# Performance work log

Measured on AMD Instinct MI355X. Metric: run time of the kernel, lower is better.

Reference implementation:

```python
import jax, jax.numpy as jnp
import numpy as np

EMB = 768
HEADS = 3
HD = EMB // HEADS  # 256
B, S = 4, 2048


def setup_inputs() -> dict:
    key = jax.random.key(0)
    ks = jax.random.split(key, 8)
    inputs_for_keys = jax.random.normal(ks[0], (B, S, EMB), dtype=jnp.float32)
    inputs_for_values = jax.random.normal(ks[1], (B, S, EMB), dtype=jnp.float32)
    inputs_for_queries = jax.random.normal(ks[2], (B, S, EMB), dtype=jnp.float32)
    # stacked per-head projection weights: [heads, emb, head_dim]
    # original uses 'random_uniform' init (small uniform); scale ~0.05
    Wk = jax.random.uniform(ks[3], (HEADS, EMB, HD), jnp.float32, -0.05, 0.05)
    Wv = jax.random.uniform(ks[4], (HEADS, EMB, HD), jnp.float32, -0.05, 0.05)
    Wq = jax.random.uniform(ks[5], (HEADS, EMB, HD), jnp.float32, -0.05, 0.05)
    Wo = jax.random.normal(ks[6], (EMB, EMB), dtype=jnp.float32) * (1.0 / np.sqrt(EMB))
    bo = jnp.zeros((EMB,), dtype=jnp.float32)
    return {
        "inputs_for_keys": inputs_for_keys,
        "inputs_for_values": inputs_for_values,
        "inputs_for_queries": inputs_for_queries,
        "Wk": Wk, "Wv": Wv, "Wq": Wq, "Wo": Wo, "bo": bo,
    }


def reference(inputs_for_keys, inputs_for_values, inputs_for_queries, Wk, Wv, Wq, Wo, bo):
    # per-head projections, batched over heads: [b, h, s, f]
    K = jnp.einsum('bse,hef->bhsf', inputs_for_keys, Wk)
    V = jnp.einsum('bse,hef->bhsf', inputs_for_values, Wv)
    Q = jnp.einsum('bse,hef->bhsf', inputs_for_queries, Wq)

    seq_k = inputs_for_keys.shape[1]
    seq_q = inputs_for_queries.shape[1]
    # NOTE: original scales by sqrt(window_size_keys) (seq len), not sqrt(d_k)
    scale = jnp.sqrt(jnp.float32(seq_k))

    scores = jnp.einsum('bhqf,bhkf->bhqk', Q, K) / scale
    # causal mask: -inf strictly above the diagonal (j > i)
    mask = jnp.triu(jnp.full((seq_q, seq_k), -jnp.inf, dtype=scores.dtype), k=1)
    scores = scores + mask

    attn = jax.nn.softmax(scores, axis=-1)  # [b,h,q,k]
    heads = jnp.einsum('bhqk,bhkf->bhqf', attn, V)

    # concat heads along feature dim: [b, q, heads*hd]
    b, h, q, f = heads.shape
    concat = heads.transpose(0, 2, 1, 3).reshape(b, q, h * f)
    return concat @ Wo + bo
```

## Files before the change

### kernel.cpp

```cpp
#include <hip/hip_runtime.h>

#define BATCH 4
#define NHEADS 3
#define SEQ 2048
#define HDIM 256
#define EMBD 768
#define MTOT (BATCH*SEQ)
#define WSZ (NHEADS*EMBD*HDIM)

typedef unsigned short u16x8 __attribute__((ext_vector_type(8)));
typedef unsigned short u16x4 __attribute__((ext_vector_type(4)));
typedef __bf16 bf16x8 __attribute__((ext_vector_type(8)));
typedef float fx4 __attribute__((ext_vector_type(4)));

__device__ __forceinline__ unsigned short f2bf(float x) {
    union { float f; unsigned int u; } v; v.f = x;
    unsigned int r = v.u + 0x7fffu + ((v.u >> 16) & 1u);
    return (unsigned short)(r >> 16);
}

__device__ __forceinline__ fx4 mfma16(u16x8 a, u16x8 b, fx4 c) {
    return __builtin_amdgcn_mfma_f32_16x16x32_bf16(
        __builtin_bit_cast(bf16x8, a), __builtin_bit_cast(bf16x8, b), c, 0, 0, 0);
}

__device__ __forceinline__ void gl_lds16(const unsigned short* g, unsigned short* l) {
    __builtin_amdgcn_global_load_lds(
        (const __attribute__((address_space(1))) unsigned int*)g,
        (__attribute__((address_space(3))) unsigned int*)l, 16, 0, 0);
}

__device__ const unsigned char attn_sched[48] = {
    124,125, 63, 120,121, 116,117, 59, 112,113, 108,109, 55, 104,105,
    100,101, 51,  96, 97,  92, 93, 47,  88, 89,  84, 85, 43,  80, 81,
     76, 77, 39,  72, 73,  68, 69, 35,  64, 65,  31, 27, 23, 19, 15,
     11,  7,  3
};

__global__ __launch_bounds__(256) void castAw_kernel(
    const float* __restrict__ Ak, const float* __restrict__ Av,
    const float* __restrict__ Aq,
    const float* __restrict__ Wk, const float* __restrict__ Wv,
    const float* __restrict__ Wq, const float* __restrict__ Wo,
    unsigned short* __restrict__ Abf, unsigned short* __restrict__ Wt,
    unsigned short* __restrict__ Wot)
{
    __shared__ float tile[64][65];
    int bx = blockIdx.x;
    if (bx < 9216) {
        int e = (bx * 256 + threadIdx.x) * 8;
        int t = e / (MTOT * EMBD);
        int r = e - t * (MTOT * EMBD);
        const float* A = (t == 0) ? Ak : (t == 1) ? Av : Aq;
        const fx4* s = (const fx4*)(A + r);
        fx4 v0 = s[0], v1 = s[1];
        u16x8 o;
        o[0]=f2bf(v0[0]); o[1]=f2bf(v0[1]); o[2]=f2bf(v0[2]); o[3]=f2bf(v0[3]);
        o[4]=f2bf(v1[0]); o[5]=f2bf(v1[1]); o[6]=f2bf(v1[2]); o[7]=f2bf(v1[3]);
        *(u16x8*)(Abf + e) = o;
        return;
    }
    int z = bx - 9216;
    const float* src; unsigned short* dst;
    int src_ld, dst_ld, e0, f0;
    if (z < 432) {
        int t = z / 144, rem = z - t * 144;
        int h = rem / 48, tl = rem - h * 48;
        e0 = (tl % 12) * 64; f0 = (tl / 12) * 64;
        const float* W = (t == 0) ? Wk : (t == 1) ? Wv : Wq;
        src = W + h * 768 * 256; src_ld = 256;
        dst = Wt + t * WSZ + h * 256 * 768; dst_ld = 768;
    } else {
        int zz = z - 432;
        e0 = (zz % 12) * 64; f0 = (zz / 12) * 64;
        src = Wo; src_ld = 768;
        dst = Wot; dst_ld = 768;
    }
    int tx = threadIdx.x & 63, ty4 = threadIdx.x >> 6;
    #pragma unroll
    for (int i = 0; i < 16; ++i) {
        int r = ty4 + i * 4;
        tile[r][tx] = src[(e0 + r) * src_ld + f0 + tx];
    }
    __syncthreads();
    #pragma unroll
    for (int i = 0; i < 16; ++i) {
        int r = ty4 + i * 4;
        dst[(f0 + r) * dst_ld + e0 + tx] = f2bf(tile[tx][r]);
    }
}

__global__ __launch_bounds__(256) void proj_kernel(
    const unsigned short* __restrict__ Abf, const unsigned short* __restrict__ Wt,
    unsigned short* __restrict__ Kg, unsigned short* __restrict__ Vg,
    unsigned short* __restrict__ Qg)
{
    __shared__ alignas(16) unsigned short S[17408];
    unsigned short* As = S;
    unsigned short* Bs = S + 8192;

    int z = blockIdx.z;
    const unsigned short* A = Abf + z * (MTOT * EMBD);
    int m0 = blockIdx.x * 128;
    int h = blockIdx.y >> 1, fbase = (blockIdx.y & 1) * 128;
    const unsigned short* W = Wt + z * WSZ + (h * 256 + fbase) * EMBD;

    int tid = threadIdx.x;
    int w = tid >> 6, ln = tid & 63;
    int lane16 = ln & 15, quad = ln >> 4;
    int mw = (w & 1) * 64, nw = (w >> 1) * 64;

    fx4 acc[4][4];
    #pragma unroll
    for (int i = 0; i < 4; ++i)
        #pragma unroll
        for (int j = 0; j < 4; ++j) acc[i][j] = (fx4){0.f, 0.f, 0.f, 0.f};

    int c0 = tid, c1 = tid + 256;
    int r0 = c0 >> 2, s0_ = (c0 & 3) * 8;
    int r1 = c1 >> 2, s1_ = (c1 & 3) * 8;
    const unsigned short* Ag0 = A + (m0 + r0) * EMBD + s0_;
    const unsigned short* Ag1 = A + (m0 + r1) * EMBD + s1_;
    const unsigned short* Wg0 = W + r0 * EMBD + s0_;
    const unsigned short* Wg1 = W + r1 * EMBD + s1_;

    for (int kb = 0; kb < EMBD; kb += 32) {
        __syncthreads();
        gl_lds16(Ag0 + kb, &As[c0 * 8]);
        gl_lds16(Ag1 + kb, &As[c1 * 8]);
        gl_lds16(Wg0 + kb, &Bs[c0 * 8]);
        gl_lds16(Wg1 + kb, &Bs[c1 * 8]);
        __syncthreads();

        u16x8 af[4], bf[4];
        #pragma unroll
        for (int i = 0; i < 4; ++i) {
            af[i] = *(const u16x8*)&As[(mw + i * 16 + lane16) * 32 + quad * 8];
            bf[i] = *(const u16x8*)&Bs[(nw + i * 16 + lane16) * 32 + quad * 8];
        }
        #pragma unroll
        for (int i = 0; i < 4; ++i)
            #pragma unroll
            for (int j = 0; j < 4; ++j)
                acc[i][j] = mfma16(af[i], bf[j], acc[i][j]);
    }

    __syncthreads();
    int b = m0 >> 11, sq0 = m0 & 2047;

    if (z == 1) {
        #pragma unroll
        for (int i = 0; i < 4; ++i)
            #pragma unroll
            for (int j = 0; j < 4; ++j) {
                int fl = nw + j * 16 + lane16;
                int ml = mw + i * 16 + quad * 4;
                u16x4 pk;
                pk[0] = f2bf(acc[i][j][0]); pk[1] = f2bf(acc[i][j][1]);
                pk[2] = f2bf(acc[i][j][2]); pk[3] = f2bf(acc[i][j][3]);
                *(u16x4*)&S[fl * 136 + ml] = pk;
            }
        __syncthreads();
        int fl = tid >> 1, mseg = (tid & 1) * 64;
        const unsigned short* srcp = &S[fl * 136 + mseg];
        unsigned short* dstp = Vg + ((b * NHEADS + h) * HDIM + fbase + fl) * SEQ + sq0 + mseg;
        #pragma unroll
        for (int c = 0; c < 8; ++c)
            *(u16x8*)(dstp + c * 8) = *(const u16x8*)(srcp + c * 8);
    } else {
        #pragma unroll
        for (int i = 0; i < 4; ++i)
            #pragma unroll
            for (int j = 0; j < 4; ++j) {
                int fl = nw + j * 16 + lane16;
                int ml = mw + i * 16 + quad * 4;
                #pragma unroll
                for (int r = 0; r < 4; ++r)
                    S[(ml + r) * 136 + fl] = f2bf(acc[i][j][r]);
            }
        __syncthreads();
        unsigned short* dst0 = (z == 0) ? Kg : Qg;
        int ml = tid >> 1, fseg = (tid & 1) * 64;
        const unsigned short* srcp = &S[ml * 136 + fseg];
        unsigned short* dstp = dst0 + ((b * NHEADS + h) * SEQ + sq0 + ml) * HDIM + fbase + fseg;
        #pragma unroll
        for (int c = 0; c < 8; ++c)
            *(u16x8*)(dstp + c * 8) = *(const u16x8*)(srcp + c * 8);
    }
}

__global__ __launch_bounds__(256) void attn_kernel(
    const unsigned short* __restrict__ Kg, const unsigned short* __restrict__ Vg,
    const unsigned short* __restrict__ Qg, unsigned short* __restrict__ heads,
    float* __restrict__ Opart, float* __restrict__ Lpart)
{
    __shared__ alignas(16) unsigned short Ks[32 * 264];
    __shared__ alignas(16) unsigned short Vs[256 * 40];

    int bx = blockIdx.x;
    int bh = bx % 12;
    int ent = attn_sched[bx / 12];
    int qt = ent >> 2, kc = ent & 3;
    int tid = threadIdx.x;
    int w = tid >> 6, ln = tid & 63;
    int lane16 = ln & 15, quad = ln >> 4;
    int q0w = qt * 64 + w * 16;

    const unsigned short* Kbase = Kg + bh * (SEQ * HDIM);
    const unsigned short* Vbase = Vg + bh * (SEQ * HDIM);
    const unsigned short* Qbase = Qg + bh * (SEQ * HDIM);

    u16x8 qf[8];
    {
        const unsigned short* qrow = Qbase + (q0w + lane16) * HDIM + quad * 8;
        #pragma unroll
        for (int c = 0; c < 8; ++c) qf[c] = *(const u16x8*)(qrow + c * 32);
    }

    fx4 o[16];
    #pragma unroll
    for (int i = 0; i < 16; ++i) o[i] = (fx4){0.f, 0.f, 0.f, 0.f};
    float lsum = 0.f;

    const float Cs2 = 0.03188010519640429f;

    int t0, t1;
    if (kc == 3) { t0 = 0; t1 = 2 * qt + 2; }
    else         { t0 = kc * (qt + 1); t1 = t0 + qt + 1; }

    int ksrow = tid >> 3, kseg = tid & 7;
    const unsigned short* kstage = Kbase + ksrow * HDIM + kseg * 32;
    const unsigned short* vstage = Vbase + tid * SEQ;

    u16x8 kreg[4], vreg[4];
    {
        int k0 = t0 * 32;
        #pragma unroll
        for (int j = 0; j < 4; ++j) {
            kreg[j] = *(const u16x8*)(kstage + k0 * HDIM + j * 8);
            vreg[j] = *(const u16x8*)(vstage + k0 + j * 8);
        }
    }

    for (int kt = t0; kt < t1; ++kt) {
        __syncthreads();
        {
            u16x8* kd = (u16x8*)&Ks[ksrow * 264 + kseg * 32];
            kd[0] = kreg[0]; kd[1] = kreg[1]; kd[2] = kreg[2]; kd[3] = kreg[3];
            u16x8* vd = (u16x8*)&Vs[tid * 40];
            vd[0] = vreg[0]; vd[1] = vreg[1]; vd[2] = vreg[2]; vd[3] = vreg[3];
        }
        if (kt + 1 < t1) {
            int k0n = (kt + 1) * 32;
            #pragma unroll
            for (int j = 0; j < 4; ++j) {
                kreg[j] = *(const u16x8*)(kstage + k0n * HDIM + j * 8);
                vreg[j] = *(const u16x8*)(vstage + k0n + j * 8);
            }
        }
        __syncthreads();

        int k0 = kt * 32;
        fx4 s0 = (fx4){0.f,0.f,0.f,0.f}, s1 = (fx4){0.f,0.f,0.f,0.f};
        #pragma unroll
        for (int c = 0; c < 8; ++c) {
            u16x8 ka = *(const u16x8*)&Ks[lane16 * 264 + c * 32 + quad * 8];
            u16x8 kb = *(const u16x8*)&Ks[(16 + lane16) * 264 + c * 32 + quad * 8];
            s0 = mfma16(ka, qf[c], s0);
            s1 = mfma16(kb, qf[c], s1);
        }

        float p0[4], p1[4];
        int q = q0w + lane16;
        #pragma unroll
        for (int r = 0; r < 4; ++r) {
            int ka_ = k0 + quad * 4 + r;
            float e0 = exp2f(s0[r] * Cs2);
            float e1 = exp2f(s1[r] * Cs2);
            p0[r] = (ka_      <= q) ? e0 : 0.f;
            p1[r] = (ka_ + 16 <= q) ? e1 : 0.f;
            lsum += p0[r] + p1[r];
        }

        u16x8 pf;
        #pragma unroll
        for (int j = 0; j < 8; ++j) {
            int srcLane = ((((quad << 1) + (j >> 2)) & 3) << 4) | lane16;
            float v0 = __shfl(p0[j & 3], srcLane, 64);
            float v1 = __shfl(p1[j & 3], srcLane, 64);
            pf[j] = f2bf(quad >= 2 ? v1 : v0);
        }

        #pragma unroll
        for (int ft = 0; ft < 16; ++ft) {
            u16x8 vf = *(const u16x8*)&Vs[(ft * 16 + lane16) * 40 + quad * 8];
            o[ft] = mfma16(pf, vf, o[ft]);
        }
    }

    lsum += __shfl_xor(lsum, 16, 64);
    lsum += __shfl_xor(lsum, 32, 64);

    if (kc == 3) {
        float linv = 1.f / lsum;
        float inv[4];
        #pragma unroll
        for (int r = 0; r < 4; ++r) inv[r] = __shfl(linv, quad * 4 + r, 64);
        int b = bh / 3, h = bh - (bh / 3) * 3;
        unsigned short* hp = heads + (b * SEQ + q0w + quad * 4) * EMBD + h * HDIM + lane16;
        #pragma unroll
        for (int ft = 0; ft < 16; ++ft)
            #pragma unroll
            for (int r = 0; r < 4; ++r)
                hp[r * EMBD + ft * 16] = f2bf(o[ft][r] * inv[r]);
    } else {
        int slot = (bh * 16 + (qt - 16)) * 2 + kc;
        float* Op = Opart + slot * 16384 + (w * 16 + quad * 4) * 256 + lane16;
        #pragma unroll
        for (int ft = 0; ft < 16; ++ft)
            #pragma unroll
            for (int r = 0; r < 4; ++r)
                Op[r * 256 + ft * 16] = o[ft][r];
        if (quad == 0) Lpart[slot * 64 + w * 16 + lane16] = lsum;
    }
}

__global__ __launch_bounds__(256) void combine_kernel(
    const float* __restrict__ Opart, const float* __restrict__ Lpart,
    unsigned short* __restrict__ heads)
{
    int t = blockIdx.x;
    int bh = t >> 4, qt = (t & 15) + 16;
    int s0 = t * 2, s1 = s0 + 1;
    int tid = threadIdx.x;
    int row = tid >> 2, fseg = (tid & 3) * 64;
    float l = Lpart[s0 * 64 + row] + Lpart[s1 * 64 + row];
    float inv = 1.f / l;
    const fx4* O0 = (const fx4*)(Opart + s0 * 16384 + row * 256 + fseg);
    const fx4* O1 = (const fx4*)(Opart + s1 * 16384 + row * 256 + fseg);
    int b = bh / 3, h = bh - (bh / 3) * 3;
    unsigned short* hp = heads + (b * SEQ + qt * 64 + row) * EMBD + h * HDIM + fseg;
    #pragma unroll
    for (int i = 0; i < 16; ++i) {
        fx4 v = O0[i] + O1[i];
        u16x4 pk;
        pk[0] = f2bf(v[0] * inv); pk[1] = f2bf(v[1] * inv);
        pk[2] = f2bf(v[2] * inv); pk[3] = f2bf(v[3] * inv);
        *(u16x4*)(hp + i * 4) = pk;
    }
}

__global__ __launch_bounds__(256) void outproj_kernel(
    const unsigned short* __restrict__ A, const unsigned short* __restrict__ Wot,
    const float* __restrict__ bo, float* __restrict__ out)
{
    __shared__ alignas(16) unsigned short S[16384];
    unsigned short* As = S;
    unsigned short* Bs = S + 8192;

    int m0 = blockIdx.x * 128, n0 = blockIdx.y * 128;
    int tid = threadIdx.x;
    int w = tid >> 6, ln = tid & 63;
    int lane16 = ln & 15, quad = ln >> 4;
    int mw = (w & 1) * 64, nw = (w >> 1) * 64;

    fx4 acc[4][4];
    #pragma unroll
    for (int i = 0; i < 4; ++i)
        #pragma unroll
        for (int j = 0; j < 4; ++j) acc[i][j] = (fx4){0.f, 0.f, 0.f, 0.f};

    int c0 = tid, c1 = tid + 256;
    int r0 = c0 >> 2, s0_ = (c0 & 3) * 8;
    int r1 = c1 >> 2, s1_ = (c1 & 3) * 8;
    const unsigned short* Ag0 = A + (m0 + r0) * EMBD + s0_;
    const unsigned short* Ag1 = A + (m0 + r1) * EMBD + s1_;
    const unsigned short* Wg0 = Wot + (n0 + r0) * EMBD + s0_;
    const unsigned short* Wg1 = Wot + (n0 + r1) * EMBD + s1_;

    for (int kb = 0; kb < EMBD; kb += 32) {
        __syncthreads();
        gl_lds16(Ag0 + kb, &As[c0 * 8]);
        gl_lds16(Ag1 + kb, &As[c1 * 8]);
        gl_lds16(Wg0 + kb, &Bs[c0 * 8]);
        gl_lds16(Wg1 + kb, &Bs[c1 * 8]);
        __syncthreads();

        u16x8 af[4], bf[4];
        #pragma unroll
        for (int i = 0; i < 4; ++i) {
            af[i] = *(const u16x8*)&As[(mw + i * 16 + lane16) * 32 + quad * 8];
            bf[i] = *(const u16x8*)&Bs[(nw + i * 16 + lane16) * 32 + quad * 8];
        }
        #pragma unroll
        for (int i = 0; i < 4; ++i)
            #pragma unroll
            for (int j = 0; j < 4; ++j)
                acc[i][j] = mfma16(af[i], bf[j], acc[i][j]);
    }

    #pragma unroll
    for (int i = 0; i < 4; ++i) {
        int mb = m0 + mw + i * 16 + quad * 4;
        #pragma unroll
        for (int j = 0; j < 4; ++j) {
            int n = n0 + nw + j * 16 + lane16;
            float bias = bo[n];
            #pragma unroll
            for (int r = 0; r < 4; ++r)
                out[(mb + r) * EMBD + n] = acc[i][j][r] + bias;
        }
    }
}

extern "C" void kernel_launch(void* const* d_in, const int* in_sizes, int n_in,
                              void* d_out, int out_size, void* d_ws, size_t ws_size,
                              hipStream_t stream) {
    const float* Ak = (const float*)d_in[0];
    const float* Av = (const float*)d_in[1];
    const float* Aq = (const float*)d_in[2];
    const float* Wk = (const float*)d_in[3];
    const float* Wv = (const float*)d_in[4];
    const float* Wq = (const float*)d_in[5];
    const float* Wo = (const float*)d_in[6];
    const float* bo = (const float*)d_in[7];
    float* out = (float*)d_out;

    char* base = (char*)d_ws;
    unsigned short* Wt    = (unsigned short*)(base);
    unsigned short* Wot   = (unsigned short*)(base + 3538944);
    unsigned short* Abf   = (unsigned short*)(base + 4718592);
    unsigned short* Kg    = (unsigned short*)(base + 42467328);
    unsigned short* Vg    = (unsigned short*)(base + 55050240);
    unsigned short* Qg    = (unsigned short*)(base + 67633152);
    unsigned short* heads = (unsigned short*)(base + 80216064);
    float* Opart = (float*)(base + 4718592);
    float* Lpart = (float*)(base + 4718592 + 25165824);

    castAw_kernel<<<dim3(9792), dim3(256), 0, stream>>>(
        Ak, Av, Aq, Wk, Wv, Wq, Wo, Abf, Wt, Wot);
    proj_kernel<<<dim3(64, 6, 3), dim3(256), 0, stream>>>(
        Abf, Wt, Kg, Vg, Qg);
    attn_kernel<<<dim3(576), dim3(256), 0, stream>>>(
        Kg, Vg, Qg, heads, Opart, Lpart);
    combine_kernel<<<dim3(192), dim3(256), 0, stream>>>(Opart, Lpart, heads);
    outproj_kernel<<<dim3(64, 6), dim3(256), 0, stream>>>(heads, Wot, bo, out);
}
```

Baseline: 292.8 us.

## Use 64-key tiles with direct global-to-LDS loads in attention kernel

Doubles the key/value tile per iteration from 32 to 64 and drops the register-staged prefetch in favour of direct global-to-LDS loads (gl_lds16) into unpadded shared arrays. The causal tile ranges and the split between partial chunks are recomputed for the larger tile. The aim is fewer barriers per key and less VGPR staging traffic. In exchange it loses the overlap between the next tile's loads and current compute, and the unpadded 512-byte and 128-byte LDS row strides may cause bank conflicts on fragment reads.

```diff
diff --git a/kernel.cpp b/kernel.cpp
--- a/kernel.cpp
+++ b/kernel.cpp
@@ -194,8 +194,8 @@
     const unsigned short* __restrict__ Qg, unsigned short* __restrict__ heads,
     float* __restrict__ Opart, float* __restrict__ Lpart)
 {
-    __shared__ alignas(16) unsigned short Ks[32 * 264];
-    __shared__ alignas(16) unsigned short Vs[256 * 40];
+    __shared__ alignas(16) unsigned short Ks[64 * 256];
+    __shared__ alignas(16) unsigned short Vs[256 * 64];
 
     int bx = blockIdx.x;
     int bh = bx % 12;
@@ -225,76 +225,65 @@
     const float Cs2 = 0.03188010519640429f;
 
     int t0, t1;
-    if (kc == 3) { t0 = 0; t1 = 2 * qt + 2; }
-    else         { t0 = kc * (qt + 1); t1 = t0 + qt + 1; }
-
-    int ksrow = tid >> 3, kseg = tid & 7;
-    const unsigned short* kstage = Kbase + ksrow * HDIM + kseg * 32;
-    const unsigned short* vstage = Vbase + tid * SEQ;
-
-    u16x8 kreg[4], vreg[4];
-    {
-        int k0 = t0 * 32;
-        #pragma unroll
-        for (int j = 0; j < 4; ++j) {
-            kreg[j] = *(const u16x8*)(kstage + k0 * HDIM + j * 8);
-            vreg[j] = *(const u16x8*)(vstage + k0 + j * 8);
+    if (kc == 3) { t0 = 0; t1 = qt + 1; }
+    else         { int half = (qt + 1) >> 1;
+                   t0 = kc ? half : 0; t1 = kc ? qt + 1 : half; }
+
+    const unsigned short* kgp = Kbase + (tid >> 5) * HDIM + (tid & 31) * 8;
+    const unsigned short* vgp = Vbase + (tid >> 3) * SEQ + (tid & 7) * 8;
+    unsigned short* ksl = &Ks[tid * 8];
+    unsigned short* vsl = &Vs[tid * 8];
+
+    for (int kt = t0; kt < t1; ++kt) {
+        int k0 = kt * 64;
+        __syncthreads();
+        #pragma unroll
+        for (int j = 0; j < 8; ++j)
+            gl_lds16(kgp + (k0 + j * 8) * HDIM, ksl + j * 2048);
+        #pragma unroll
+        for (int j = 0; j < 8; ++j)
+            gl_lds16(vgp + j * 32 * SEQ + k0, vsl + j * 2048);
+        __syncthreads();
+
+        fx4 sacc[4];
+        #pragma unroll
+        for (int ks = 0; ks < 4; ++ks) sacc[ks] = (fx4){0.f,0.f,0.f,0.f};
+        #pragma unroll
+        for (int c = 0; c < 8; ++c) {
+            #pragma unroll
+            for (int ks = 0; ks < 4; ++ks) {
+                u16x8 kf = *(const u16x8*)&Ks[(ks * 16 + lane16) * 256 + c * 32 + quad * 8];
+                sacc[ks] = mfma16(kf, qf[c], sacc[ks]);
+            }
         }
-    }
-
-    for (int kt = t0; kt < t1; ++kt) {
-        __syncthreads();
-        {
-            u16x8* kd = (u16x8*)&Ks[ksrow * 264 + kseg * 32];
-            kd[0] = kreg[0]; kd[1] = kreg[1]; kd[2] = kreg[2]; kd[3] = kreg[3];
-            u16x8* vd = (u16x8*)&Vs[tid * 40];
-            vd[0] = vreg[0]; vd[1] = vreg[1]; vd[2] = vreg[2]; vd[3] = vreg[3];
-        }
-        if (kt + 1 < t1) {
-            int k0n = (kt + 1) * 32;
-            #pragma unroll
-            for (int j = 0; j < 4; ++j) {
-                kreg[j] = *(const u16x8*)(kstage + k0n * HDIM + j * 8);
-                vreg[j] = *(const u16x8*)(vstage + k0n + j * 8);
-            }
-        }
-        __syncthreads();
-
-        int k0 = kt * 32;
-        fx4 s0 = (fx4){0.f,0.f,0.f,0.f}, s1 = (fx4){0.f,0.f,0.f,0.f};
-        #pragma unroll
-        for (int c = 0; c < 8; ++c) {
-            u16x8 ka = *(const u16x8*)&Ks[lane16 * 264 + c * 32 + quad * 8];
-            u16x8 kb = *(const u16x8*)&Ks[(16 + lane16) * 264 + c * 32 + quad * 8];
-            s0 = mfma16(ka, qf[c], s0);
-            s1 = mfma16(kb, qf[c], s1);
-        }
-
-        float p0[4], p1[4];
+
+        float p[4][4];
         int q = q0w + lane16;
         #pragma unroll
-        for (int r = 0; r < 4; ++r) {
-            int ka_ = k0 + quad * 4 + r;
-            float e0 = exp2f(s0[r] * Cs2);
-            float e1 = exp2f(s1[r] * Cs2);
-            p0[r] = (ka_      <= q) ? e0 : 0.f;
-            p1[r] = (ka_ + 16 <= q) ? e1 : 0.f;
-            lsum += p0[r] + p1[r];
-        }
-
-        u16x8 pf;
-        #pragma unroll
-        for (int j = 0; j < 8; ++j) {
-            int srcLane = ((((quad << 1) + (j >> 2)) & 3) << 4) | lane16;
-            float v0 = __shfl(p0[j & 3], srcLane, 64);
-            float v1 = __shfl(p1[j & 3], srcLane, 64);
-            pf[j] = f2bf(quad >= 2 ? v1 : v0);
-        }
-
-        #pragma unroll
-        for (int ft = 0; ft < 16; ++ft) {
-            u16x8 vf = *(const u16x8*)&Vs[(ft * 16 + lane16) * 40 + quad * 8];
-            o[ft] = mfma16(pf, vf, o[ft]);
+        for (int ks = 0; ks < 4; ++ks)
+            #pragma unroll
+            for (int r = 0; r < 4; ++r) {
+                int ka_ = k0 + ks * 16 + quad * 4 + r;
+                float e = exp2f(sacc[ks][r] * Cs2);
+                p[ks][r] = (ka_ <= q) ? e : 0.f;
+                lsum += p[ks][r];
+            }
+
+        #pragma unroll
+        for (int hh = 0; hh < 2; ++hh) {
+            u16x8 pf;
+            #pragma unroll
+            for (int j = 0; j < 8; ++j) {
+                int srcLane = ((((quad << 1) + (j >> 2)) & 3) << 4) | lane16;
+                float v0 = __shfl(p[2 * hh][j & 3], srcLane, 64);
+                float v1 = __shfl(p[2 * hh + 1][j & 3], srcLane, 64);
+                pf[j] = f2bf(quad >= 2 ? v1 : v0);
+            }
+            #pragma unroll
+            for (int ft = 0; ft < 16; ++ft) {
+                u16x8 vf = *(const u16x8*)&Vs[(ft * 16 + lane16) * 64 + hh * 32 + quad * 8];
+                o[ft] = mfma16(pf, vf, o[ft]);
+            }
         }
     }
 
```

Measured after the change: 323.6 us. 1.11x slower.
